# Performance work log

Measured on AMD Instinct MI355X. Metric: run time of the kernel, lower is better.

The kernel has to match this reference:

```python
import jax, jax.numpy as jnp
import numpy as np

N_HEADS = 4
ITERS = 3
EPS = 1e-8


def layer_norm(x, g, b, eps=1e-5):
    m = jnp.mean(x, axis=-1, keepdims=True)
    v = jnp.mean((x - m) ** 2, axis=-1, keepdims=True)
    return (x - m) * jax.lax.rsqrt(v + eps) * g + b


def gru_cell(x, h, Wih, Whh, bih, bhh):
    # PyTorch GRUCell semantics. x: [M, kvq], h: [M, dim]
    gi = x @ Wih.T + bih
    gh = h @ Whh.T + bhh
    ir, iz, i_n = jnp.split(gi, 3, axis=-1)
    hr, hz, h_n = jnp.split(gh, 3, axis=-1)
    r = jax.nn.sigmoid(ir + hr)
    z = jax.nn.sigmoid(iz + hz)
    n = jnp.tanh(i_n + r * h_n)
    return (1.0 - z) * n + z * h


def slot_attention(features, slots, Wq, Wk, Wv, g_in, b_in, g_s, b_s, Wih, Whh, bih, bhh):
    b, n, _ = features.shape
    _, ns, dim = slots.shape
    kvq = Wk.shape[0]
    dh = kvq // N_HEADS
    scale = dh ** -0.5
    inp = layer_norm(features, g_in, b_in)
    k = (inp @ Wk.T).reshape(b, n, N_HEADS, dh)
    v = (inp @ Wv.T).reshape(b, n, N_HEADS, dh)
    attn_vis = None
    for _ in range(ITERS):
        slots_prev = slots
        s = layer_norm(slots, g_s, b_s)
        q = (s @ Wq.T).reshape(b, ns, N_HEADS, dh)
        dots = jnp.einsum("bihd,bjhd->bihj", q, k) * scale
        attn = jax.nn.softmax(dots, axis=1)  # competitive softmax over slots
        attn_vis = attn.mean(axis=2)  # [b, ns, n]
        w = attn + EPS
        w = w / jnp.sum(w, axis=-1, keepdims=True)  # weighted mean over features
        upd = jnp.einsum("bjhd,bihj->bihd", v, w).reshape(b, ns, kvq)
        slots = gru_cell(upd.reshape(-1, kvq), slots_prev.reshape(-1, dim),
                         Wih, Whh, bih, bhh).reshape(b, ns, dim)
    return slots, attn_vis


def vq_pool(x, codebook):
    # x: [b, ns, d], codebook: [C, d]
    d2 = (jnp.sum(x ** 2, axis=-1, keepdims=True)
          - 2.0 * jnp.einsum("bnd,cd->bnc", x, codebook)
          + jnp.sum(codebook ** 2, axis=-1))
    idx = jnp.argmin(d2, axis=-1)
    q = codebook[idx]
    commit = jnp.mean((x - jax.lax.stop_gradient(q)) ** 2)
    q = x + jax.lax.stop_gradient(q - x)  # straight-through
    return q, idx, commit


def setup_inputs() -> dict:
    key = jax.random.key(0)
    ks = jax.random.split(key, 16)
    B, N, FD = 32, 1024, 768
    NS, D, KVQ, C = 24, 256, 256, 512
    sc = lambda d: d ** -0.5
    return {
        "features": jax.random.normal(ks[0], (B, N, FD), jnp.float32),
        "conditioning": jax.random.normal(ks[1], (B, NS, D), jnp.float32),
        "Wq": jax.random.normal(ks[2], (KVQ, D), jnp.float32) * sc(D),
        "Wk": jax.random.normal(ks[3], (KVQ, FD), jnp.float32) * sc(FD),
        "Wv": jax.random.normal(ks[4], (KVQ, FD), jnp.float32) * sc(FD),
        "g_in": jnp.ones((FD,), jnp.float32),
        "b_in": jnp.zeros((FD,), jnp.float32),
        "g_s": jnp.ones((D,), jnp.float32),
        "b_s": jnp.zeros((D,), jnp.float32),
        "Wih": jax.random.normal(ks[5], (3 * D, KVQ), jnp.float32) * sc(KVQ),
        "Whh": jax.random.normal(ks[6], (3 * D, D), jnp.float32) * sc(D),
        "bih": jnp.zeros((3 * D,), jnp.float32),
        "bhh": jnp.zeros((3 * D,), jnp.float32),
        "codebook": jax.random.normal(ks[7], (C, D), jnp.float32) * sc(D),
    }


def reference(features, conditioning, Wq, Wk, Wv, g_in, b_in, g_s, b_s,
              Wih, Whh, bih, bhh, codebook):
    sa = lambda f, s: slot_attention(f, s, Wq, Wk, Wv, g_in, b_in, g_s, b_s,
                                     Wih, Whh, bih, bhh)
    slots, pre_attn = sa(features, conditioning)
    q_slots, indices, commit = vq_pool(slots, codebook)
    slots, post_attn = sa(features, q_slots)
    return slots, post_attn, pre_attn, indices, commit
```

## Files before the change

kernel.cpp:

```cpp
#include <hip/hip_runtime.h>
#include <math.h>

#define LB __launch_bounds__(256)

constexpr int BATCH = 32, NFEAT = 1024, FDIM = 768, NSLOT = 24;
constexpr int NH = 4, DH = 64, NITER = 3;
constexpr int MF = BATCH * NFEAT;
constexpr int MS = BATCH * NSLOT;
constexpr float QSCALE = 0.125f;
constexpr float ATTN_EPS = 1e-8f;
constexpr float LNEPS = 1e-5f;

typedef __attribute__((ext_vector_type(8))) short bf16x8;
typedef __attribute__((ext_vector_type(4))) float f32x4;

__device__ __forceinline__ unsigned short f2bf(float x) {
  unsigned u = __float_as_uint(x);
  return (unsigned short)((u + 0x7FFFu + ((u >> 16) & 1u)) >> 16);
}
__device__ __forceinline__ float bf2f(unsigned short h) {
  return __uint_as_float(((unsigned)h) << 16);
}
__device__ __forceinline__ void cvt8(const float4& a, const float4& b, float m, float r,
                                     int4& hi, int4& lo) {
  float v[8] = {a.x, a.y, a.z, a.w, b.x, b.y, b.z, b.w};
  unsigned sh[8], sl[8];
#pragma unroll
  for (int j = 0; j < 8; ++j) {
    float vv = (v[j] - m) * r;
    unsigned short h = f2bf(vv);
    sh[j] = h;
    sl[j] = f2bf(vv - bf2f(h));
  }
  hi = make_int4((int)(sh[0] | (sh[1] << 16)), (int)(sh[2] | (sh[3] << 16)),
                 (int)(sh[4] | (sh[5] << 16)), (int)(sh[6] | (sh[7] << 16)));
  lo = make_int4((int)(sl[0] | (sl[1] << 16)), (int)(sl[2] | (sl[3] << 16)),
                 (int)(sl[4] | (sl[5] << 16)), (int)(sl[6] | (sl[7] << 16)));
}

__device__ __forceinline__ void gll16(const void* g, void* l) {
  __builtin_amdgcn_global_load_lds(
      (const __attribute__((address_space(1))) void*)g,
      (__attribute__((address_space(3))) void*)l, 16, 0, 0);
}

__global__ LB void k_preprow(const float* __restrict__ x, float* __restrict__ stats,
                             const float* __restrict__ Wk, const float* __restrict__ Wv,
                             const float* __restrict__ Wq,
                             const float* __restrict__ g_in, const float* __restrict__ b_in,
                             const float* __restrict__ g_s, const float* __restrict__ b_s,
                             short* __restrict__ Bh_g, short* __restrict__ Bl_g,
                             short* __restrict__ Wgqh, short* __restrict__ Wgql,
                             float* __restrict__ cconst) {
  const int t = threadIdx.x;
  if (blockIdx.x < MF / 4) {
    const int row = blockIdx.x * 4 + (t >> 6);
    const int lane = t & 63;
    const float* xr = x + (size_t)row * FDIM;
    float s = 0.f, sq = 0.f;
#pragma unroll
    for (int i = 0; i < 3; ++i) {
      float4 v = *(const float4*)(xr + i * 256 + lane * 4);
      s += v.x + v.y + v.z + v.w;
      sq += v.x * v.x + v.y * v.y + v.z * v.z + v.w * v.w;
    }
#pragma unroll
    for (int o = 32; o > 0; o >>= 1) { s += __shfl_down(s, o, 64); sq += __shfl_down(sq, o, 64); }
    if (lane == 0) {
      float m = s / (float)FDIM;
      float var = sq / (float)FDIM - m * m;
      stats[row * 2] = m;
      stats[row * 2 + 1] = 1.f / sqrtf(var + LNEPS);
    }
    return;
  }
  const int r = blockIdx.x - MF / 4;
  float s = 0.f;
  if (r < 512) {
    const float* srcW = (r < 256) ? (Wk + (size_t)r * FDIM) : (Wv + (size_t)(r - 256) * FDIM);
    for (int k = t; k < FDIM; k += 256) {
      float w = srcW[k];
      float wg = w * g_in[k];
      s += b_in[k] * w;
      unsigned short h = f2bf(wg);
      Bh_g[(size_t)r * FDIM + k] = (short)h;
      Bl_g[(size_t)r * FDIM + k] = (short)f2bf(wg - bf2f(h));
    }
  } else {
    const int c = r - 512;
    float w = Wq[(size_t)c * 256 + t];
    float wg = w * g_s[t];
    unsigned short hh = f2bf(wg);
    Wgqh[(size_t)c * 256 + t] = (short)hh;
    Wgql[(size_t)c * 256 + t] = (short)f2bf(wg - bf2f(hh));
    s = b_s[t] * w;
  }
  __shared__ float red[256];
  red[t] = s; __syncthreads();
  for (int o = 128; o > 0; o >>= 1) { if (t < o) red[t] += red[t + o]; __syncthreads(); }
  if (t == 0) cconst[r] = red[0];
}

__global__ LB void k_mfkv(const float* __restrict__ x, const float* __restrict__ stats,
                          const short* __restrict__ Bh_g, const short* __restrict__ Bl_g,
                          const float* __restrict__ cconst,
                          short* __restrict__ khi, short* __restrict__ klo,
                          short* __restrict__ vThi, short* __restrict__ vTlo) {
  __shared__ short Ah[2048], Al[2048];
  __shared__ short Bh[2][4096], Bl[2][4096];
  const int t = threadIdx.x;
  const int l = t & 63;
  const int w = t >> 6;
  const int row0 = blockIdx.x * 64;
  const int c0 = blockIdx.y * 128;

  const int sAr = t >> 2;
  const int sl = t & 3;
  const int kqA = sl ^ ((sAr >> 1) & 3);
  const float* pa = x + (size_t)(row0 + sAr) * FDIM + kqA * 8;
  const float mA = stats[(row0 + sAr) * 2], rA = stats[(row0 + sAr) * 2 + 1];
  const int sBr1 = sAr + 64;
  const int kqB1 = sl ^ ((sBr1 >> 1) & 3);
  const short* pkh0 = Bh_g + (size_t)(c0 + sAr) * FDIM + kqA * 8;
  const short* pkh1 = Bh_g + (size_t)(c0 + sBr1) * FDIM + kqB1 * 8;
  const short* pkl0 = Bl_g + (size_t)(c0 + sAr) * FDIM + kqA * 8;
  const short* pkl1 = Bl_g + (size_t)(c0 + sBr1) * FDIM + kqB1 * 8;
  const short* pvh0 = Bh_g + (size_t)(256 + c0 + sAr) * FDIM + kqA * 8;
  const short* pvh1 = Bh_g + (size_t)(256 + c0 + sBr1) * FDIM + kqB1 * 8;
  const short* pvl0 = Bl_g + (size_t)(256 + c0 + sAr) * FDIM + kqA * 8;
  const short* pvl1 = Bl_g + (size_t)(256 + c0 + sBr1) * FDIM + kqB1 * 8;
  const int wbA = t * 16;
  const int wb0 = t * 16, wb1 = (t + 256) * 16;

  const int wm = (w >> 1) * 32, wn = (w & 1) * 64;
  int aoff[2], boff[4];
#pragma unroll
  for (int m = 0; m < 2; ++m) {
    const int ar = wm + m * 16 + (l & 15);
    const int kq = l >> 4;
    aoff[m] = ar * 64 + ((kq ^ ((ar >> 1) & 3)) << 4);
  }
#pragma unroll
  for (int n = 0; n < 4; ++n) {
    const int bc = wn + n * 16 + (l & 15);
    const int kq = l >> 4;
    boff[n] = bc * 64 + ((kq ^ ((bc >> 1) & 3)) << 4);
  }

  f32x4 acc[2][2][4] = {};
  float4 raa = *(const float4*)pa, rab = *(const float4*)(pa + 4);

  for (int s = 0; s < FDIM / 32; ++s) {
    if (s) __syncthreads();
    const int ko = s * 32;
    gll16(pkh0 + ko, (char*)&Bh[0][0] + wb0);
    gll16(pkh1 + ko, (char*)&Bh[0][0] + wb1);
    gll16(pkl0 + ko, (char*)&Bl[0][0] + wb0);
    gll16(pkl1 + ko, (char*)&Bl[0][0] + wb1);
    gll16(pvh0 + ko, (char*)&Bh[1][0] + wb0);
    gll16(pvh1 + ko, (char*)&Bh[1][0] + wb1);
    gll16(pvl0 + ko, (char*)&Bl[1][0] + wb0);
    gll16(pvl1 + ko, (char*)&Bl[1][0] + wb1);
    int4 hi, lo;
    cvt8(raa, rab, mA, rA, hi, lo);
    *(int4*)((char*)Ah + wbA) = hi; *(int4*)((char*)Al + wbA) = lo;
    if (s + 1 < FDIM / 32) {
      raa = *(const float4*)(pa + ko + 32);
      rab = *(const float4*)(pa + ko + 36);
    }
    __syncthreads();
    bf16x8 fah[2], fal[2];
#pragma unroll
    for (int m = 0; m < 2; ++m) {
      fah[m] = *(const bf16x8*)((const char*)Ah + aoff[m]);
      fal[m] = *(const bf16x8*)((const char*)Al + aoff[m]);
    }
#pragma unroll
    for (int kv = 0; kv < 2; ++kv) {
      bf16x8 fbh[4], fbl[4];
#pragma unroll
      for (int n = 0; n < 4; ++n) {
        fbh[n] = *(const bf16x8*)((const char*)&Bh[kv][0] + boff[n]);
        fbl[n] = *(const bf16x8*)((const char*)&Bl[kv][0] + boff[n]);
      }
#pragma unroll
      for (int m = 0; m < 2; ++m)
#pragma unroll
        for (int n = 0; n < 4; ++n) {
          acc[kv][m][n] = __builtin_amdgcn_mfma_f32_16x16x32_bf16(fal[m], fbh[n], acc[kv][m][n], 0, 0, 0);
          acc[kv][m][n] = __builtin_amdgcn_mfma_f32_16x16x32_bf16(fah[m], fbl[n], acc[kv][m][n], 0, 0, 0);
          acc[kv][m][n] = __builtin_amdgcn_mfma_f32_16x16x32_bf16(fah[m], fbh[n], acc[kv][m][n], 0, 0, 0);
        }
    }
  }
  const int b_blk = row0 >> 10;
  const int jbase = row0 & 1023;
#pragma unroll
  for (int m = 0; m < 2; ++m) {
    const int rloc = wm + m * 16 + ((l >> 4) << 2);
    const int rbase = row0 + rloc;
#pragma unroll
    for (int n = 0; n < 4; ++n) {
      const int col = c0 + wn + n * 16 + (l & 15);
      const float cck = cconst[col];
      const float ccv = cconst[256 + col];
      const int hh2 = col >> 6, dh = col & 63;
      const size_t vrow = ((size_t)(b_blk * 4 + hh2) * 64 + dh) * 1024;
#pragma unroll
      for (int r = 0; r < 4; ++r) {
        const float kval = acc[0][m][n][r] + cck;
        const unsigned short h = f2bf(kval);
        khi[(size_t)(rbase + r) * 256 + col] = (short)h;
        klo[(size_t)(rbase + r) * 256 + col] = (short)f2bf(kval - bf2f(h));
        const float vval = acc[1][m][n][r] + ccv;
        const unsigned short hv = f2bf(vval);
        vThi[vrow + jbase + rloc + r] = (short)hv;
        vTlo[vrow + jbase + rloc + r] = (short)f2bf(vval - bf2f(hv));
      }
    }
  }
}

template <bool WRITE_ATTN>
__global__ LB void k_fdots(const float* __restrict__ slots,
                           const short* __restrict__ Wgqh, const short* __restrict__ Wgql,
                           const float* __restrict__ cconst,
                           const short* __restrict__ khi, const short* __restrict__ klo,
                           const short* __restrict__ vThi, const short* __restrict__ vTlo,
                           float* __restrict__ attn, float* __restrict__ updp,
                           float* __restrict__ ssump) {
  const int blk = blockIdx.x;
  const int jc = blk & 3;
  const int h = (blk >> 2) & 3;
  const int b = blk >> 4;
  const int t = threadIdx.x;
  const int l = t & 63;
  const int w = t >> 6;
  __shared__ float sc[24 * 256];
  __shared__ short sh_[32 * 256];
  __shared__ short sl_[32 * 256];
  __shared__ short qh[2048], ql[2048];
  __shared__ float part[4][NSLOT];
  __shared__ float mst[NSLOT], rst[NSLOT];

  if (t < 192) {
    const int r = t >> 3, g = t & 7;
    const float* sr = slots + (size_t)(b * NSLOT + r) * 256 + g * 32;
    float s = 0.f, sq = 0.f;
#pragma unroll
    for (int m4 = 0; m4 < 8; ++m4) {
      float4 v = *(const float4*)(sr + m4 * 4);
      *(float4*)&sc[r * 256 + g * 32 + m4 * 4] = v;
      s += v.x + v.y + v.z + v.w;
      sq += v.x * v.x + v.y * v.y + v.z * v.z + v.w * v.w;
    }
    s += __shfl_down(s, 4, 8); sq += __shfl_down(sq, 4, 8);
    s += __shfl_down(s, 2, 8); sq += __shfl_down(sq, 2, 8);
    s += __shfl_down(s, 1, 8); sq += __shfl_down(sq, 1, 8);
    if (g == 0) {
      float mm = s * (1.f / 256.f);
      mst[r] = mm;
      rst[r] = 1.f / sqrtf(sq * (1.f / 256.f) - mm * mm + LNEPS);
    }
  }
  __syncthreads();
#pragma unroll 4
  for (int i = 0; i < NSLOT; ++i) {
    const float v = (sc[i * 256 + t] - mst[i]) * rst[i];
    const unsigned short hh = f2bf(v);
    const int slot = i * 32 + ((t >> 3) ^ (i & 31));
    sh_[slot * 8 + (t & 7)] = (short)hh;
    sl_[slot * 8 + (t & 7)] = (short)f2bf(v - bf2f(hh));
  }
  __syncthreads();
  {
    f32x4 qacc[2] = {};
#pragma unroll
    for (int ks = 0; ks < 8; ++ks) {
      bf16x8 ah[2], al[2];
#pragma unroll
      for (int m = 0; m < 2; ++m) {
        const int row = m * 16 + (l & 15);
        const int g = ks * 4 + (l >> 4);
        const int slot = row * 32 + (g ^ (row & 31));
        ah[m] = *(const bf16x8*)&sh_[slot * 8];
        al[m] = *(const bf16x8*)&sl_[slot * 8];
      }
      const size_t brow = (size_t)(h * 64 + w * 16 + (l & 15)) * 256 + ks * 32 + (l >> 4) * 8;
      const bf16x8 bh = *(const bf16x8*)(Wgqh + brow);
      const bf16x8 bl2 = *(const bf16x8*)(Wgql + brow);
#pragma unroll
      for (int m = 0; m < 2; ++m) {
        qacc[m] = __builtin_amdgcn_mfma_f32_16x16x32_bf16(al[m], bh, qacc[m], 0, 0, 0);
        qacc[m] = __builtin_amdgcn_mfma_f32_16x16x32_bf16(ah[m], bl2, qacc[m], 0, 0, 0);
        qacc[m] = __builtin_amdgcn_mfma_f32_16x16x32_bf16(ah[m], bh, qacc[m], 0, 0, 0);
      }
    }
    const int d = w * 16 + (l & 15);
    const float qc = cconst[512 + h * 64 + d];
#pragma unroll
    for (int m = 0; m < 2; ++m)
#pragma unroll
      for (int r = 0; r < 4; ++r) {
        const int row = m * 16 + (l >> 4) * 4 + r;
        const float qv = qacc[m][r] + qc;
        const unsigned short hh = f2bf(qv);
        const int slot = row * 8 + ((d >> 3) ^ (row & 7));
        qh[slot * 8 + (d & 7)] = (short)hh;
        ql[slot * 8 + (d & 7)] = (short)f2bf(qv - bf2f(hh));
      }
  }
  __syncthreads();
  {
    const short* khb = khi + (size_t)(b * NFEAT + jc * 256) * 256 + h * 64;
    const short* klb = klo + (size_t)(b * NFEAT + jc * 256) * 256 + h * 64;
    f32x4 scc[2][4] = {};
#pragma unroll
    for (int ks = 0; ks < 2; ++ks) {
      bf16x8 ah[2], al[2];
#pragma unroll
      for (int m = 0; m < 2; ++m) {
        const int row = m * 16 + (l & 15);
        const int g = ks * 4 + (l >> 4);
        const int slot = row * 8 + (g ^ (row & 7));
        ah[m] = *(const bf16x8*)&qh[slot * 8];
        al[m] = *(const bf16x8*)&ql[slot * 8];
      }
#pragma unroll
      for (int nl = 0; nl < 4; ++nl) {
        const int nt = w * 4 + nl;
        const size_t boffg = (size_t)(nt * 16 + (l & 15)) * 256 + ks * 32 + (l >> 4) * 8;
        const bf16x8 bh = *(const bf16x8*)(khb + boffg);
        const bf16x8 bl2 = *(const bf16x8*)(klb + boffg);
#pragma unroll
        for (int m = 0; m < 2; ++m) {
          scc[m][nl] = __builtin_amdgcn_mfma_f32_16x16x32_bf16(al[m], bh, scc[m][nl], 0, 0, 0);
          scc[m][nl] = __builtin_amdgcn_mfma_f32_16x16x32_bf16(ah[m], bl2, scc[m][nl], 0, 0, 0);
          scc[m][nl] = __builtin_amdgcn_mfma_f32_16x16x32_bf16(ah[m], bh, scc[m][nl], 0, 0, 0);
        }
      }
    }
#pragma unroll
    for (int m = 0; m < 2; ++m)
#pragma unroll
      for (int nl = 0; nl < 4; ++nl) {
        const int col = (w * 4 + nl) * 16 + (l & 15);
        const int rbase = m * 16 + ((l >> 4) << 2);
#pragma unroll
        for (int r = 0; r < 4; ++r)
          if (rbase + r < 24) sc[(rbase + r) * 256 + col] = scc[m][nl][r];
      }
  }
  __syncthreads();
  {
    float acc[NSLOT];
#pragma unroll
    for (int i = 0; i < NSLOT; ++i) acc[i] = sc[i * 256 + t];
    float mx = -1e30f;
#pragma unroll
    for (int i = 0; i < NSLOT; ++i) { acc[i] *= QSCALE; mx = fmaxf(mx, acc[i]); }
    float s = 0.f;
#pragma unroll
    for (int i = 0; i < NSLOT; ++i) { acc[i] = expf(acc[i] - mx); s += acc[i]; }
    const float inv = 1.f / s;
    float* ab = attn + (size_t)(b * NH + h) * NSLOT * NFEAT + jc * 256 + t;
#pragma unroll
    for (int i = 0; i < NSLOT; ++i) {
      const float wgt = acc[i] * inv;
      if (WRITE_ATTN) ab[(size_t)i * NFEAT] = wgt;
      const float ae = wgt + ATTN_EPS;
      acc[i] = ae;
      const unsigned short hh = f2bf(ae);
      const int slot = i * 32 + ((t >> 3) ^ (i & 31));
      sh_[slot * 8 + (t & 7)] = (short)hh;
      sl_[slot * 8 + (t & 7)] = (short)f2bf(ae - bf2f(hh));
    }
#pragma unroll
    for (int i = 0; i < NSLOT; ++i) {
      float rs = acc[i];
#pragma unroll
      for (int o = 32; o > 0; o >>= 1) rs += __shfl_down(rs, o, 64);
      if (l == 0) part[w][i] = rs;
    }
  }
  __syncthreads();
  {
    f32x4 pacc[2] = {};
#pragma unroll
    for (int ks = 0; ks < 8; ++ks) {
      bf16x8 ah[2], al[2];
#pragma unroll
      for (int m = 0; m < 2; ++m) {
        const int row = m * 16 + (l & 15);
        const int g = ks * 4 + (l >> 4);
        const int slot = row * 32 + (g ^ (row & 31));
        ah[m] = *(const bf16x8*)&sh_[slot * 8];
        al[m] = *(const bf16x8*)&sl_[slot * 8];
      }
      const size_t brow = ((size_t)(b * 4 + h) * 64 + w * 16 + (l & 15)) * 1024 +
                          jc * 256 + ks * 32 + (l >> 4) * 8;
      const bf16x8 bh = *(const bf16x8*)(vThi + brow);
      const bf16x8 bl2 = *(const bf16x8*)(vTlo + brow);
#pragma unroll
      for (int m = 0; m < 2; ++m) {
        pacc[m] = __builtin_amdgcn_mfma_f32_16x16x32_bf16(al[m], bh, pacc[m], 0, 0, 0);
        pacc[m] = __builtin_amdgcn_mfma_f32_16x16x32_bf16(ah[m], bl2, pacc[m], 0, 0, 0);
        pacc[m] = __builtin_amdgcn_mfma_f32_16x16x32_bf16(ah[m], bh, pacc[m], 0, 0, 0);
      }
    }
    const int d = w * 16 + (l & 15);
    float* up = updp + (size_t)((b * 4 + h) * 4 + jc) * NSLOT * 64;
#pragma unroll
    for (int m = 0; m < 2; ++m)
#pragma unroll
      for (int r = 0; r < 4; ++r) {
        const int row = m * 16 + (l >> 4) * 4 + r;
        if (row < 24) up[row * 64 + d] = pacc[m][r];
      }
  }
  if (t < NSLOT)
    ssump[((size_t)(b * 4 + h) * 4 + jc) * NSLOT + t] =
        part[0][t] + part[1][t] + part[2][t] + part[3][t];
}

template <bool FINAL>
__global__ LB void k_grufin(const float* __restrict__ updp, const float* __restrict__ ssump,
                            const float* __restrict__ sprev,
                            const float* __restrict__ Wih, const float* __restrict__ Whh,
                            const float* __restrict__ bih, const float* __restrict__ bhh,
                            float* __restrict__ snext, float* __restrict__ outs) {
  __shared__ float updt[8][256];
  __shared__ float Bs[3][16][33];
  const int bx = blockIdx.x;
  const int d0 = blockIdx.y * 32;
  const int rows0 = bx * 8;
  const int t = threadIdx.x;
  {
    const int h = t >> 6, d = t & 63;
#pragma unroll
    for (int u = 0; u < 8; ++u) {
      const int row = rows0 + u;
      const int b = row / 24, i = row - b * 24;
      const size_t base = (size_t)(b * 4 + h) * 4;
      float s = 0.f, wsum = 0.f;
#pragma unroll
      for (int jc = 0; jc < 4; ++jc) {
        s += updp[(base + jc) * (NSLOT * 64) + i * 64 + d];
        wsum += ssump[(base + jc) * NSLOT + i];
      }
      updt[u][h * 64 + d] = s / wsum;
    }
  }
  __syncthreads();
  const int r = t >> 5;
  const int dd = t & 31;
  float accR = 0.f, accZ = 0.f, accN = 0.f, accH = 0.f;
  for (int k0 = 0; k0 < 256; k0 += 16) {
    {
      int i = t;
      {
        const int s = i >> 7, rem = i & 127, c = rem >> 2, kq = rem & 3;
        float4 wv = *(const float4*)(Wih + (size_t)(s * 256 + d0 + c) * 256 + k0 + kq * 4);
        Bs[s][kq * 4 + 0][c] = wv.x; Bs[s][kq * 4 + 1][c] = wv.y;
        Bs[s][kq * 4 + 2][c] = wv.z; Bs[s][kq * 4 + 3][c] = wv.w;
      }
      if (t < 128) {
        i = 256 + t;
        const int s = i >> 7, rem = i & 127, c = rem >> 2, kq = rem & 3;
        float4 wv = *(const float4*)(Wih + (size_t)(s * 256 + d0 + c) * 256 + k0 + kq * 4);
        Bs[s][kq * 4 + 0][c] = wv.x; Bs[s][kq * 4 + 1][c] = wv.y;
        Bs[s][kq * 4 + 2][c] = wv.z; Bs[s][kq * 4 + 3][c] = wv.w;
      }
    }
    __syncthreads();
#pragma unroll
    for (int kk = 0; kk < 16; ++kk) {
      const float a = updt[r][k0 + kk];
      accR += a * Bs[0][kk][dd];
      accZ += a * Bs[1][kk][dd];
      accN += a * Bs[2][kk][dd];
    }
    __syncthreads();
  }
  {
    const int rr2 = t >> 5, c0 = (t & 31) * 8;
    const float* sp = sprev + (size_t)(rows0 + rr2) * 256 + c0;
    *(float4*)&updt[rr2][c0] = *(const float4*)sp;
    *(float4*)&updt[rr2][c0 + 4] = *(const float4*)(sp + 4);
  }
  __syncthreads();
  for (int k0 = 0; k0 < 256; k0 += 16) {
    {
      int i = t;
      {
        const int s = i >> 7, rem = i & 127, c = rem >> 2, kq = rem & 3;
        float4 wv = *(const float4*)(Whh + (size_t)(s * 256 + d0 + c) * 256 + k0 + kq * 4);
        Bs[s][kq * 4 + 0][c] = wv.x; Bs[s][kq * 4 + 1][c] = wv.y;
        Bs[s][kq * 4 + 2][c] = wv.z; Bs[s][kq * 4 + 3][c] = wv.w;
      }
      if (t < 128) {
        i = 256 + t;
        const int s = i >> 7, rem = i & 127, c = rem >> 2, kq = rem & 3;
        float4 wv = *(const float4*)(Whh + (size_t)(s * 256 + d0 + c) * 256 + k0 + kq * 4);
        Bs[s][kq * 4 + 0][c] = wv.x; Bs[s][kq * 4 + 1][c] = wv.y;
        Bs[s][kq * 4 + 2][c] = wv.z; Bs[s][kq * 4 + 3][c] = wv.w;
      }
    }
    __syncthreads();
#pragma unroll
    for (int kk = 0; kk < 16; ++kk) {
      const float a = updt[r][k0 + kk];
      accR += a * Bs[0][kk][dd];
      accZ += a * Bs[1][kk][dd];
      accH += a * Bs[2][kk][dd];
    }
    __syncthreads();
  }
  const int row = rows0 + r;
  const int c = d0 + dd;
  const float hp = updt[r][c];
  const float rr = 1.f / (1.f + expf(-(accR + bih[c] + bhh[c])));
  const float zz = 1.f / (1.f + expf(-(accZ + bih[256 + c] + bhh[256 + c])));
  const float nn = tanhf(accN + bih[512 + c] + rr * (accH + bhh[512 + c]));
  const float o = (1.f - zz) * nn + zz * hp;
  snext[(size_t)row * 256 + c] = o;
  if (FINAL) outs[(size_t)row * 256 + c] = o;
}

__global__ LB void k_attnvis(const float* __restrict__ attn, float* __restrict__ out) {
  const int idx = blockIdx.x * 256 + threadIdx.x;
  const int j = idx & 1023;
  const int rem = idx >> 10;
  const int i = rem % NSLOT;
  const int b = rem / NSLOT;
  float s = 0.f;
#pragma unroll
  for (int h = 0; h < NH; ++h)
    s += attn[(size_t)((b * NH + h) * NSLOT + i) * NFEAT + j];
  out[idx] = 0.25f * s;
}

__global__ LB void k_vqvis(float* __restrict__ slots, const float* __restrict__ cb,
                           const float* __restrict__ attn,
                           float* __restrict__ idx_out, float* __restrict__ bestd2,
                           float* __restrict__ vis_out) {
  const int t = threadIdx.x;
  if (blockIdx.x >= MS) {
    const int idx = (blockIdx.x - MS) * 256 + t;
    const int j = idx & 1023;
    const int rem = idx >> 10;
    const int i = rem % NSLOT;
    const int b = rem / NSLOT;
    float s = 0.f;
#pragma unroll
    for (int h = 0; h < NH; ++h)
      s += attn[(size_t)((b * NH + h) * NSLOT + i) * NFEAT + j];
    vis_out[idx] = 0.25f * s;
    return;
  }
  const int r = blockIdx.x;
  __shared__ float xs[256];
  __shared__ float red[256];
  __shared__ float rv[256];
  __shared__ int ri[256];
  xs[t] = slots[(size_t)r * 256 + t];
  __syncthreads();
  red[t] = xs[t] * xs[t]; __syncthreads();
  for (int o = 128; o > 0; o >>= 1) { if (t < o) red[t] += red[t + o]; __syncthreads(); }
  const float x2 = red[0];
  float best = 1e30f; int bidx = 0;
#pragma unroll
  for (int cset = 0; cset < 2; ++cset) {
    const int c = cset * 256 + t;
    const float* cr = cb + (size_t)c * 256;
    float xc = 0.f, cc = 0.f;
    for (int dd = 0; dd < 256; dd += 4) {
      float4 cv = *(const float4*)(cr + dd);
      xc += xs[dd] * cv.x + xs[dd + 1] * cv.y + xs[dd + 2] * cv.z + xs[dd + 3] * cv.w;
      cc += cv.x * cv.x + cv.y * cv.y + cv.z * cv.z + cv.w * cv.w;
    }
    float d2 = x2 - 2.f * xc + cc;
    if (d2 < best) { best = d2; bidx = c; }
  }
  rv[t] = best; ri[t] = bidx; __syncthreads();
  for (int o = 128; o > 0; o >>= 1) {
    if (t < o) {
      if (rv[t + o] < rv[t] || (rv[t + o] == rv[t] && ri[t + o] < ri[t])) {
        rv[t] = rv[t + o]; ri[t] = ri[t + o];
      }
    }
    __syncthreads();
  }
  const int wi = ri[0];
  const float cval = cb[(size_t)wi * 256 + t];
  const float diff = xs[t] - cval;
  red[t] = diff * diff; __syncthreads();
  for (int o = 128; o > 0; o >>= 1) { if (t < o) red[t] += red[t + o]; __syncthreads(); }
  if (t == 0) { idx_out[r] = (float)wi; bestd2[r] = red[0]; }
  slots[(size_t)r * 256 + t] = cval;
}

__global__ LB void k_commit(const float* __restrict__ bestd2, float* __restrict__ out) {
  const int t = threadIdx.x;
  __shared__ float red[256];
  float s = 0.f;
  for (int i = t; i < MS; i += 256) s += bestd2[i];
  red[t] = s; __syncthreads();
  for (int o = 128; o > 0; o >>= 1) { if (t < o) red[t] += red[t + o]; __syncthreads(); }
  if (t == 0) out[0] = red[0] / (float)(MS * 256);
}

extern "C" void kernel_launch(void* const* d_in, const int* in_sizes, int n_in,
                              void* d_out, int out_size, void* d_ws, size_t ws_size,
                              hipStream_t stream) {
  const float* features = (const float*)d_in[0];
  const float* cond = (const float*)d_in[1];
  const float* Wq = (const float*)d_in[2];
  const float* Wk = (const float*)d_in[3];
  const float* Wv = (const float*)d_in[4];
  const float* g_in = (const float*)d_in[5];
  const float* b_in = (const float*)d_in[6];
  const float* g_s = (const float*)d_in[7];
  const float* b_s = (const float*)d_in[8];
  const float* Wih = (const float*)d_in[9];
  const float* Whh = (const float*)d_in[10];
  const float* bih = (const float*)d_in[11];
  const float* bhh = (const float*)d_in[12];
  const float* cb = (const float*)d_in[13];
  float* out = (float*)d_out;

  char* wsb = (char*)d_ws;
  short* Bh_g = (short*)wsb; wsb += (size_t)512 * FDIM * 2;
  short* Bl_g = (short*)wsb; wsb += (size_t)512 * FDIM * 2;
  short* khi = (short*)wsb; wsb += (size_t)MF * 256 * 2;
  short* klo = (short*)wsb; wsb += (size_t)MF * 256 * 2;
  short* vThi = (short*)wsb; wsb += (size_t)MF * 256 * 2;
  short* vTlo = (short*)wsb; wsb += (size_t)MF * 256 * 2;
  short* Wgqh = (short*)wsb; wsb += (size_t)256 * 256 * 2;
  short* Wgql = (short*)wsb; wsb += (size_t)256 * 256 * 2;
  float* ws = (float*)wsb;
  float* stats = ws;  ws += 2 * MF;
  float* attn = ws;   ws += (size_t)BATCH * NH * NSLOT * NFEAT;
  float* sbufA = ws;  ws += (size_t)MS * 256;
  float* sbufB = ws;  ws += (size_t)MS * 256;
  float* updp = ws;   ws += (size_t)512 * NSLOT * 64;
  float* ssump = ws;  ws += (size_t)512 * NSLOT;
  float* cconst = ws; ws += 768;
  float* bestd2 = ws; ws += MS;

  float* out_slots = out;
  float* out_post = out + 196608;
  float* out_pre = out + 196608 + 786432;
  float* out_idx = out + 196608 + 786432 * 2;
  float* out_commit = out_idx + 768;

  k_preprow<<<MF / 4 + 768, 256, 0, stream>>>(features, stats, Wk, Wv, Wq, g_in, b_in,
                                              g_s, b_s, Bh_g, Bl_g, Wgqh, Wgql, cconst);
  k_mfkv<<<dim3(MF / 64, 2), 256, 0, stream>>>(features, stats, Bh_g, Bl_g, cconst,
                                               khi, klo, vThi, vTlo);

  const float* scur = cond;
  float* bufs[2] = {sbufA, sbufB};
  int nb = 0;
  for (int call = 0; call < 2; ++call) {
    for (int it = 0; it < NITER; ++it) {
      float* snxt = bufs[nb]; nb ^= 1;
      if (it == NITER - 1)
        k_fdots<true><<<512, 256, 0, stream>>>(scur, Wgqh, Wgql, cconst, khi, klo,
                                               vThi, vTlo, attn, updp, ssump);
      else
        k_fdots<false><<<512, 256, 0, stream>>>(scur, Wgqh, Wgql, cconst, khi, klo,
                                                vThi, vTlo, attn, updp, ssump);
      if (call == 1 && it == NITER - 1)
        k_grufin<true><<<dim3(MS / 8, 8), 256, 0, stream>>>(updp, ssump, scur, Wih, Whh,
                                                            bih, bhh, snxt, out_slots);
      else
        k_grufin<false><<<dim3(MS / 8, 8), 256, 0, stream>>>(updp, ssump, scur, Wih, Whh,
                                                             bih, bhh, snxt, out_slots);
      scur = snxt;
    }
    if (call == 0) {
      k_vqvis<<<MS + BATCH * NSLOT * NFEAT / 256, 256, 0, stream>>>(
          (float*)scur, cb, attn, out_idx, bestd2, out_pre);
      k_commit<<<1, 256, 0, stream>>>(bestd2, out_commit);
    } else {
      k_attnvis<<<BATCH * NSLOT * NFEAT / 256, 256, 0, stream>>>(attn, out_post);
    }
  }
}
```

Before: 557.7 us.

## Stage V transpose in LDS, widen GRU K tiles, fuse attn-vis into final GRU

The K/V projection epilogue now stages the transposed V tile in shared memory, unioned with the GEMM buffers, and writes vThi/vTlo with coalesced 16-byte stores instead of scattered 2-byte stores. The GRU kernel loads 64-wide K tiles of Wih/Whh per sync instead of 16-wide, which cuts barrier count at the cost of more shared memory. The final post-attention head-mean is folded into the last GRU launch, which removes one kernel launch but puts extra memory work on that kernel's threads.

```diff
diff --git a/kernel.cpp b/kernel.cpp
--- a/kernel.cpp
+++ b/kernel.cpp
@@ -101,13 +101,17 @@
   if (t == 0) cconst[r] = red[0];
 }
 
+union SmemM {
+  struct { short Ah[2048], Al[2048], Bh[2][4096], Bl[2][4096]; } m;
+  struct { short vh[128][72], vl[128][72]; } e;
+};
+
 __global__ LB void k_mfkv(const float* __restrict__ x, const float* __restrict__ stats,
                           const short* __restrict__ Bh_g, const short* __restrict__ Bl_g,
                           const float* __restrict__ cconst,
                           short* __restrict__ khi, short* __restrict__ klo,
                           short* __restrict__ vThi, short* __restrict__ vTlo) {
-  __shared__ short Ah[2048], Al[2048];
-  __shared__ short Bh[2][4096], Bl[2][4096];
+  __shared__ SmemM sm;
   const int t = threadIdx.x;
   const int l = t & 63;
   const int w = t >> 6;
@@ -153,17 +157,17 @@
   for (int s = 0; s < FDIM / 32; ++s) {
     if (s) __syncthreads();
     const int ko = s * 32;
-    gll16(pkh0 + ko, (char*)&Bh[0][0] + wb0);
-    gll16(pkh1 + ko, (char*)&Bh[0][0] + wb1);
-    gll16(pkl0 + ko, (char*)&Bl[0][0] + wb0);
-    gll16(pkl1 + ko, (char*)&Bl[0][0] + wb1);
-    gll16(pvh0 + ko, (char*)&Bh[1][0] + wb0);
-    gll16(pvh1 + ko, (char*)&Bh[1][0] + wb1);
-    gll16(pvl0 + ko, (char*)&Bl[1][0] + wb0);
-    gll16(pvl1 + ko, (char*)&Bl[1][0] + wb1);
+    gll16(pkh0 + ko, (char*)&sm.m.Bh[0][0] + wb0);
+    gll16(pkh1 + ko, (char*)&sm.m.Bh[0][0] + wb1);
+    gll16(pkl0 + ko, (char*)&sm.m.Bl[0][0] + wb0);
+    gll16(pkl1 + ko, (char*)&sm.m.Bl[0][0] + wb1);
+    gll16(pvh0 + ko, (char*)&sm.m.Bh[1][0] + wb0);
+    gll16(pvh1 + ko, (char*)&sm.m.Bh[1][0] + wb1);
+    gll16(pvl0 + ko, (char*)&sm.m.Bl[1][0] + wb0);
+    gll16(pvl1 + ko, (char*)&sm.m.Bl[1][0] + wb1);
     int4 hi, lo;
     cvt8(raa, rab, mA, rA, hi, lo);
-    *(int4*)((char*)Ah + wbA) = hi; *(int4*)((char*)Al + wbA) = lo;
+    *(int4*)((char*)sm.m.Ah + wbA) = hi; *(int4*)((char*)sm.m.Al + wbA) = lo;
     if (s + 1 < FDIM / 32) {
       raa = *(const float4*)(pa + ko + 32);
       rab = *(const float4*)(pa + ko + 36);
@@ -172,16 +176,16 @@
     bf16x8 fah[2], fal[2];
 #pragma unroll
     for (int m = 0; m < 2; ++m) {
-      fah[m] = *(const bf16x8*)((const char*)Ah + aoff[m]);
-      fal[m] = *(const bf16x8*)((const char*)Al + aoff[m]);
+      fah[m] = *(const bf16x8*)((const char*)sm.m.Ah + aoff[m]);
+      fal[m] = *(const bf16x8*)((const char*)sm.m.Al + aoff[m]);
     }
 #pragma unroll
     for (int kv = 0; kv < 2; ++kv) {
       bf16x8 fbh[4], fbl[4];
 #pragma unroll
       for (int n = 0; n < 4; ++n) {
-        fbh[n] = *(const bf16x8*)((const char*)&Bh[kv][0] + boff[n]);
-        fbl[n] = *(const bf16x8*)((const char*)&Bl[kv][0] + boff[n]);
+        fbh[n] = *(const bf16x8*)((const char*)&sm.m.Bh[kv][0] + boff[n]);
+        fbl[n] = *(const bf16x8*)((const char*)&sm.m.Bl[kv][0] + boff[n]);
       }
 #pragma unroll
       for (int m = 0; m < 2; ++m)
@@ -193,6 +197,7 @@
         }
     }
   }
+  __syncthreads();
   const int b_blk = row0 >> 10;
   const int jbase = row0 & 1023;
 #pragma unroll
@@ -201,22 +206,40 @@
     const int rbase = row0 + rloc;
 #pragma unroll
     for (int n = 0; n < 4; ++n) {
-      const int col = c0 + wn + n * 16 + (l & 15);
-      const float cck = cconst[col];
-      const float ccv = cconst[256 + col];
-      const int hh2 = col >> 6, dh = col & 63;
-      const size_t vrow = ((size_t)(b_blk * 4 + hh2) * 64 + dh) * 1024;
+      const int col = wn + n * 16 + (l & 15);
+      const int gcol = c0 + col;
+      const float cck = cconst[gcol];
+      const float ccv = cconst[256 + gcol];
+      unsigned vhp[2] = {0, 0}, vlp[2] = {0, 0};
 #pragma unroll
       for (int r = 0; r < 4; ++r) {
         const float kval = acc[0][m][n][r] + cck;
         const unsigned short h = f2bf(kval);
-        khi[(size_t)(rbase + r) * 256 + col] = (short)h;
-        klo[(size_t)(rbase + r) * 256 + col] = (short)f2bf(kval - bf2f(h));
+        khi[(size_t)(rbase + r) * 256 + gcol] = (short)h;
+        klo[(size_t)(rbase + r) * 256 + gcol] = (short)f2bf(kval - bf2f(h));
         const float vval = acc[1][m][n][r] + ccv;
         const unsigned short hv = f2bf(vval);
-        vThi[vrow + jbase + rloc + r] = (short)hv;
-        vTlo[vrow + jbase + rloc + r] = (short)f2bf(vval - bf2f(hv));
-      }
+        const unsigned short lv = f2bf(vval - bf2f(hv));
+        vhp[r >> 1] |= ((unsigned)hv) << ((r & 1) * 16);
+        vlp[r >> 1] |= ((unsigned)lv) << ((r & 1) * 16);
+      }
+      *(int2*)((short*)&sm.e.vh[0][0] + col * 72 + rloc) = make_int2((int)vhp[0], (int)vhp[1]);
+      *(int2*)((short*)&sm.e.vl[0][0] + col * 72 + rloc) = make_int2((int)vlp[0], (int)vlp[1]);
+    }
+  }
+  __syncthreads();
+  {
+    const int vr = t >> 1;
+    const int vh2 = (t & 1) * 32;
+    const int gcol = c0 + vr;
+    const int hh2 = gcol >> 6, dh = gcol & 63;
+    const size_t vrow = ((size_t)(b_blk * 4 + hh2) * 64 + dh) * 1024 + jbase + vh2;
+    const short* sh2 = (const short*)&sm.e.vh[0][0] + vr * 72 + vh2;
+    const short* sl2 = (const short*)&sm.e.vl[0][0] + vr * 72 + vh2;
+#pragma unroll
+    for (int q = 0; q < 4; ++q) {
+      *(int4*)(vThi + vrow + q * 8) = *(const int4*)(sh2 + q * 8);
+      *(int4*)(vTlo + vrow + q * 8) = *(const int4*)(sl2 + q * 8);
     }
   }
 }
@@ -428,9 +451,10 @@
                             const float* __restrict__ sprev,
                             const float* __restrict__ Wih, const float* __restrict__ Whh,
                             const float* __restrict__ bih, const float* __restrict__ bhh,
-                            float* __restrict__ snext, float* __restrict__ outs) {
+                            float* __restrict__ snext, float* __restrict__ outs,
+                            const float* __restrict__ attn, float* __restrict__ vis_out) {
   __shared__ float updt[8][256];
-  __shared__ float Bs[3][16][33];
+  __shared__ float Bs[3][64][33];
   const int bx = blockIdx.x;
   const int d0 = blockIdx.y * 32;
   const int rows0 = bx * 8;
@@ -455,26 +479,18 @@
   const int r = t >> 5;
   const int dd = t & 31;
   float accR = 0.f, accZ = 0.f, accN = 0.f, accH = 0.f;
-  for (int k0 = 0; k0 < 256; k0 += 16) {
-    {
-      int i = t;
-      {
-        const int s = i >> 7, rem = i & 127, c = rem >> 2, kq = rem & 3;
-        float4 wv = *(const float4*)(Wih + (size_t)(s * 256 + d0 + c) * 256 + k0 + kq * 4);
-        Bs[s][kq * 4 + 0][c] = wv.x; Bs[s][kq * 4 + 1][c] = wv.y;
-        Bs[s][kq * 4 + 2][c] = wv.z; Bs[s][kq * 4 + 3][c] = wv.w;
-      }
-      if (t < 128) {
-        i = 256 + t;
-        const int s = i >> 7, rem = i & 127, c = rem >> 2, kq = rem & 3;
-        float4 wv = *(const float4*)(Wih + (size_t)(s * 256 + d0 + c) * 256 + k0 + kq * 4);
-        Bs[s][kq * 4 + 0][c] = wv.x; Bs[s][kq * 4 + 1][c] = wv.y;
-        Bs[s][kq * 4 + 2][c] = wv.z; Bs[s][kq * 4 + 3][c] = wv.w;
-      }
+  for (int k0 = 0; k0 < 256; k0 += 64) {
+#pragma unroll
+    for (int ii = 0; ii < 6; ++ii) {
+      const int i = ii * 256 + t;
+      const int s = i / 512, rem = i & 511, c = rem >> 4, kq = rem & 15;
+      float4 wv = *(const float4*)(Wih + (size_t)(s * 256 + d0 + c) * 256 + k0 + kq * 4);
+      Bs[s][kq * 4 + 0][c] = wv.x; Bs[s][kq * 4 + 1][c] = wv.y;
+      Bs[s][kq * 4 + 2][c] = wv.z; Bs[s][kq * 4 + 3][c] = wv.w;
     }
     __syncthreads();
 #pragma unroll
-    for (int kk = 0; kk < 16; ++kk) {
+    for (int kk = 0; kk < 64; ++kk) {
       const float a = updt[r][k0 + kk];
       accR += a * Bs[0][kk][dd];
       accZ += a * Bs[1][kk][dd];
@@ -489,26 +505,18 @@
     *(float4*)&updt[rr2][c0 + 4] = *(const float4*)(sp + 4);
   }
   __syncthreads();
-  for (int k0 = 0; k0 < 256; k0 += 16) {
-    {
-      int i = t;
-      {
-        const int s = i >> 7, rem = i & 127, c = rem >> 2, kq = rem & 3;
-        float4 wv = *(const float4*)(Whh + (size_t)(s * 256 + d0 + c) * 256 + k0 + kq * 4);
-        Bs[s][kq * 4 + 0][c] = wv.x; Bs[s][kq * 4 + 1][c] = wv.y;
-        Bs[s][kq * 4 + 2][c] = wv.z; Bs[s][kq * 4 + 3][c] = wv.w;
-      }
-      if (t < 128) {
-        i = 256 + t;
-        const int s = i >> 7, rem = i & 127, c = rem >> 2, kq = rem & 3;
-        float4 wv = *(const float4*)(Whh + (size_t)(s * 256 + d0 + c) * 256 + k0 + kq * 4);
-        Bs[s][kq * 4 + 0][c] = wv.x; Bs[s][kq * 4 + 1][c] = wv.y;
-        Bs[s][kq * 4 + 2][c] = wv.z; Bs[s][kq * 4 + 3][c] = wv.w;
-      }
+  for (int k0 = 0; k0 < 256; k0 += 64) {
+#pragma unroll
+    for (int ii = 0; ii < 6; ++ii) {
+      const int i = ii * 256 + t;
+      const int s = i / 512, rem = i & 511, c = rem >> 4, kq = rem & 15;
+      float4 wv = *(const float4*)(Whh + (size_t)(s * 256 + d0 + c) * 256 + k0 + kq * 4);
+      Bs[s][kq * 4 + 0][c] = wv.x; Bs[s][kq * 4 + 1][c] = wv.y;
+      Bs[s][kq * 4 + 2][c] = wv.z; Bs[s][kq * 4 + 3][c] = wv.w;
     }
     __syncthreads();
 #pragma unroll
-    for (int kk = 0; kk < 16; ++kk) {
+    for (int kk = 0; kk < 64; ++kk) {
       const float a = updt[r][k0 + kk];
       accR += a * Bs[0][kk][dd];
       accZ += a * Bs[1][kk][dd];
@@ -524,20 +532,23 @@
   const float nn = tanhf(accN + bih[512 + c] + rr * (accH + bhh[512 + c]));
   const float o = (1.f - zz) * nn + zz * hp;
   snext[(size_t)row * 256 + c] = o;
-  if (FINAL) outs[(size_t)row * 256 + c] = o;
-}
-
-__global__ LB void k_attnvis(const float* __restrict__ attn, float* __restrict__ out) {
-  const int idx = blockIdx.x * 256 + threadIdx.x;
-  const int j = idx & 1023;
-  const int rem = idx >> 10;
-  const int i = rem % NSLOT;
-  const int b = rem / NSLOT;
-  float s = 0.f;
-#pragma unroll
-  for (int h = 0; h < NH; ++h)
-    s += attn[(size_t)((b * NH + h) * NSLOT + i) * NFEAT + j];
-  out[idx] = 0.25f * s;
+  if (FINAL) {
+    outs[(size_t)row * 256 + c] = o;
+    const int gid = (blockIdx.y * 96 + blockIdx.x) * 256 + t;
+#pragma unroll
+    for (int z = 0; z < 4; ++z) {
+      const int idx = z * 196608 + gid;
+      const int j = idx & 1023;
+      const int rem = idx >> 10;
+      const int i = rem % NSLOT;
+      const int b = rem / NSLOT;
+      float s = 0.f;
+#pragma unroll
+      for (int hh = 0; hh < NH; ++hh)
+        s += attn[(size_t)((b * NH + hh) * NSLOT + i) * NFEAT + j];
+      vis_out[idx] = 0.25f * s;
+    }
+  }
 }
 
 __global__ LB void k_vqvis(float* __restrict__ slots, const float* __restrict__ cb,
@@ -673,18 +684,18 @@
                                                 vThi, vTlo, attn, updp, ssump);
       if (call == 1 && it == NITER - 1)
         k_grufin<true><<<dim3(MS / 8, 8), 256, 0, stream>>>(updp, ssump, scur, Wih, Whh,
-                                                            bih, bhh, snxt, out_slots);
+                                                            bih, bhh, snxt, out_slots,
+                                                            attn, out_post);
       else
         k_grufin<false><<<dim3(MS / 8, 8), 256, 0, stream>>>(updp, ssump, scur, Wih, Whh,
-                                                             bih, bhh, snxt, out_slots);
+                                                             bih, bhh, snxt, out_slots,
+                                                             nullptr, nullptr);
       scur = snxt;
     }
     if (call == 0) {
       k_vqvis<<<MS + BATCH * NSLOT * NFEAT / 256, 256, 0, stream>>>(
           (float*)scur, cb, attn, out_idx, bestd2, out_pre);
       k_commit<<<1, 256, 0, stream>>>(bestd2, out_commit);
-    } else {
-      k_attnvis<<<BATCH * NSLOT * NFEAT / 256, 256, 0, stream>>>(attn, out_post);
-    }
-  }
-}
+    }
+  }
+}
```

Result: no change. 559.9 us (+0.4%).
